# Kernel tuning notes

Hardware: AMD Instinct MI355X
Metric: run time of the kernel (lower is better)

The kernel has to match this reference:

```python
import jax, jax.numpy as jnp
from jax import lax
import numpy as np

B, T, F = 256, 2048, 12
EV_VOCAB, RS_VOCAB = 32, 8
EED, RED = 6, 3
H, K = 96, 3
D = F + EED + RED  # 21


def setup_inputs() -> dict:
    key = jax.random.key(0)
    ks = jax.random.split(key, 12)
    s = 0.05
    return {
        'seq': jax.random.normal(ks[0], (B, T, F), jnp.float32),
        'ev': jax.random.randint(ks[1], (B, T), 0, EV_VOCAB),
        'rs': jax.random.randint(ks[2], (B, T), 0, RS_VOCAB),
        'lengths': jax.random.randint(ks[3], (B,), 1, T + 1),  # valid lengths in [1, T]
        'event_emb': jax.random.normal(ks[4], (EV_VOCAB, EED), jnp.float32) * s,
        'result_emb': jax.random.normal(ks[5], (RS_VOCAB, RED), jnp.float32) * s,
        'W_ih': jax.random.normal(ks[6], (4 * H, D), jnp.float32) * s,
        'W_hh': jax.random.normal(ks[7], (4 * H, H), jnp.float32) * s,
        'b_ih': jnp.zeros((4 * H,), jnp.float32),
        'b_hh': jnp.zeros((4 * H,), jnp.float32),
        'W_mlp': jax.random.normal(ks[8], (H, H * K), jnp.float32) * s,
        'b_mlp': jnp.zeros((H,), jnp.float32),
        'W_fc': jax.random.normal(ks[9], (2, 2 * H), jnp.float32) * s,
        'b_fc': jnp.zeros((2,), jnp.float32),
    }


def reference(seq, ev, rs, lengths, event_emb, result_emb, W_ih, W_hh, b_ih, b_hh,
              W_mlp, b_mlp, W_fc, b_fc):
    # embed + concat -> [B,T,D]
    x = jnp.concatenate([seq, event_emb[ev], result_emb[rs]], axis=-1)
    xs = jnp.swapaxes(x, 0, 1)  # [T,B,D]
    ts = jnp.arange(T)
    b = b_ih + b_hh

    def step(carry, inp):
        h, c = carry
        x_t, t = inp
        gates = x_t @ W_ih.T + h @ W_hh.T + b  # [B,4H]
        i, f, g, o = jnp.split(gates, 4, axis=-1)  # PyTorch gate order i,f,g,o
        i = jax.nn.sigmoid(i); f = jax.nn.sigmoid(f)
        g = jnp.tanh(g); o = jax.nn.sigmoid(o)
        c_new = f * c + i * g
        h_new = o * jnp.tanh(c_new)
        m = (t < lengths)[:, None]  # packed-seq semantics: freeze state past length
        h = jnp.where(m, h_new, h)
        c = jnp.where(m, c_new, c)
        out = jnp.where(m, h_new, jnp.zeros_like(h_new))  # pad_packed zeros
        return (h, c), out

    h0 = jnp.zeros((B, H), x.dtype)
    (h_fin, _), outs = lax.scan(step, (h0, h0), (xs, ts))
    out_padded = jnp.swapaxes(outs, 0, 1)  # [B,T,H]

    # vectorized last-k gather (replaces torch Python loop)
    idx = lengths[:, None] - K + jnp.arange(K)  # [B,K]
    valid = idx >= 0
    gathered = jnp.take_along_axis(out_padded, jnp.clip(idx, 0)[:, :, None], axis=1)
    gathered = jnp.where(valid[:, :, None], gathered, jnp.zeros_like(gathered))
    lastk = gathered.reshape(B, K * H)

    h_lastk = jax.nn.relu(lastk @ W_mlp.T + b_mlp)
    h = jnp.concatenate([h_fin, h_lastk], axis=1)  # [B,2H]
    return h @ W_fc.T + b_fc  # [B,2]
```

## Files before the change

### kernel.cpp

```cpp
#include <hip/hip_runtime.h>

#define TT 2048
#define FF 12
#define CH 128
#define L2E 1.44269504088896340736f

typedef float v2f __attribute__((ext_vector_type(2)));

__device__ __forceinline__ float fast_exp2(float x){ return __builtin_amdgcn_exp2f(x); }
__device__ __forceinline__ float fast_rcp(float x){ return __builtin_amdgcn_rcpf(x); }
__device__ __forceinline__ v2f fma2(v2f a, v2f b, v2f c){ return __builtin_elementwise_fma(a, b, c); }
__device__ __forceinline__ v2f mk2(float x, float y){ v2f r; r.x = x; r.y = y; return r; }

__global__ __launch_bounds__(384, 2) void lstm_persist(
  const float* __restrict__ seq, const int* __restrict__ ev, const int* __restrict__ rsi,
  const int* __restrict__ len, const float* __restrict__ eemb, const float* __restrict__ remb,
  const float* __restrict__ W_ih, const float* __restrict__ W_hh,
  const float* __restrict__ b_ih, const float* __restrict__ b_hh,
  const float* __restrict__ W_mlp, const float* __restrict__ b_mlp,
  const float* __restrict__ W_fc, const float* __restrict__ b_fc,
  float* __restrict__ out)
{
  const int b   = blockIdx.x;
  const int tid = threadIdx.x;
  const int qg  = tid & 3;
  const int u   = tid >> 2;
  const int g   = qg*96 + u;

  __shared__ __align__(16) float xf[CH*24];
  __shared__ __align__(16) float vhbuf[2*96];
  __shared__ __align__(16) float lastk[3*96];
  __shared__ __align__(16) float et[192];
  __shared__ __align__(16) float rt[24];
  __shared__ __align__(16) float accs[192];
  __shared__ __align__(16) float h2[2*96];
  __shared__ int evb[CH];
  __shared__ int rsb[CH];

  v2f wh[48];
  {
    const float4* wp = (const float4*)(W_hh + g*96);
    #pragma unroll
    for (int k = 0; k < 24; ++k) {
      const float4 q4 = wp[k];
      wh[2*k]   = mk2(q4.x, q4.y);
      wh[2*k+1] = mk2(q4.z, q4.w);
    }
  }
  float wi[21];
  #pragma unroll
  for (int c = 0; c < 21; ++c) wi[c] = W_ih[g*21 + c];
  const float bg = b_ih[g] + b_hh[g];

  if (tid < 192) { vhbuf[tid] = 0.f; et[tid] = eemb[tid]; }
  if (tid < 24)  rt[tid] = remb[tid];
  if (tid < 288) lastk[tid] = 0.f;

  float c_state = 0.f;
  const int L = len[b];

  for (int t0 = 0; t0 < L; t0 += CH) {
    #pragma unroll
    for (int qq = 0; qq < 4; ++qq) {
      const int i = tid + qq*384;
      const int r = i/12, c = i - r*12;
      xf[r*24 + c] = seq[(size_t)b*(TT*FF) + (size_t)t0*FF + i];
    }
    if (tid < CH) {
      evb[tid] = ev [b*TT + t0 + tid];
      rsb[tid] = rsi[b*TT + t0 + tid];
    }
    __syncthreads();
    #pragma unroll
    for (int qq = 0; qq < 4; ++qq) {
      const int i = tid + qq*384;
      const int r = i/12, cc = i - r*12 + 12;
      float v;
      if (cc < 18)      v = et[evb[r]*6 + (cc-12)];
      else if (cc < 21) v = rt[rsb[r]*3 + (cc-18)];
      else              v = 0.f;
      xf[r*24 + cc] = v;
    }
    __syncthreads();

    const int nr = min(CH, L - t0);
    float xp;
    {
      const float* xr = xf;
      float s0 = bg, s1 = 0.f, s2 = 0.f;
      #pragma unroll
      for (int c = 0; c < 7; ++c) {
        s0 = fmaf(wi[c],    xr[c],    s0);
        s1 = fmaf(wi[c+7],  xr[c+7],  s1);
        s2 = fmaf(wi[c+14], xr[c+14], s2);
      }
      xp = s0 + s1 + s2;
    }

    for (int r = 0; r < nr; ++r) {
      const float4* hq = (const float4*)(vhbuf + (r&1)*96);
      v2f a0 = mk2(xp, 0.f), a1 = mk2(0.f,0.f), a2 = mk2(0.f,0.f), a3 = mk2(0.f,0.f);
      #pragma unroll
      for (int k = 0; k < 24; k += 2) {
        const float4 h4 = hq[k];
        const float4 h5 = hq[k+1];
        a0 = fma2(wh[2*k],   mk2(h4.x,h4.y), a0);
        a1 = fma2(wh[2*k+1], mk2(h4.z,h4.w), a1);
        a2 = fma2(wh[2*k+2], mk2(h5.x,h5.y), a2);
        a3 = fma2(wh[2*k+3], mk2(h5.z,h5.w), a3);
      }
      const float s = ((a0.x+a0.y)+(a1.x+a1.y)) + ((a2.x+a2.y)+(a3.x+a3.y));
      const bool is_t = (qg == 2);
      const float arg = is_t ? (-2.f*L2E)*fabsf(s) : (-L2E)*s;
      const float e  = fast_exp2(arg);
      const float r1 = fast_rcp(1.f + e);
      const float th = copysignf((1.f - e)*r1, s);
      const float a  = is_t ? th : r1;
      const float t1 = __shfl_xor(a, 2);
      const float t2 = __shfl_xor(a, 1);
      const float t3 = __shfl_xor(t1, 1);
      if (qg == 0) {
        c_state = fmaf(t2, c_state, a*t1);
        const float e2  = fast_exp2((-2.f*L2E)*fabsf(c_state));
        const float th2 = copysignf((1.f - e2)*fast_rcp(1.f + e2), c_state);
        const float hn  = t3 * th2;
        vhbuf[((r&1)^1)*96 + u] = hn;
        const int kk = (t0 + r) + 3 - L;
        if (kk >= 0) lastk[kk*96 + u] = hn;
      }
      if (r + 1 < nr) {
        const float* xr = xf + (r+1)*24;
        float s0 = bg, s1 = 0.f, s2 = 0.f;
        #pragma unroll
        for (int c = 0; c < 7; ++c) {
          s0 = fmaf(wi[c],    xr[c],    s0);
          s1 = fmaf(wi[c+7],  xr[c+7],  s1);
          s2 = fmaf(wi[c+14], xr[c+14], s2);
        }
        xp = s0 + s1 + s2;
      }
      __syncthreads();
    }
  }

  const float* hf = vhbuf + (L & 1)*96;
  if (tid < 192) {
    const int half = tid / 96;
    const int m    = tid - half*96;
    const float* wp = W_mlp + m*288 + half*144;
    const float* xq = lastk + half*144;
    float s = 0.f;
    #pragma unroll 8
    for (int i = 0; i < 144; ++i) s = fmaf(wp[i], xq[i], s);
    accs[tid] = s;
  }
  __syncthreads();
  if (tid < 96) {
    const float hl = accs[tid] + accs[96+tid] + b_mlp[tid];
    h2[96 + tid] = fmaxf(hl, 0.f);
    h2[tid] = hf[tid];
  }
  __syncthreads();
  if (tid < 128) {
    const int o  = tid >> 6;
    const int ll = tid & 63;
    const float* wf = W_fc + o*192 + 3*ll;
    float s = fmaf(wf[0], h2[3*ll+0], fmaf(wf[1], h2[3*ll+1], wf[2]*h2[3*ll+2]));
    #pragma unroll
    for (int off = 32; off > 0; off >>= 1) s += __shfl_down(s, off);
    if (ll == 0) out[b*2 + o] = s + b_fc[o];
  }
}

extern "C" void kernel_launch(void* const* d_in, const int* in_sizes, int n_in,
                              void* d_out, int out_size, void* d_ws, size_t ws_size,
                              hipStream_t stream) {
  const float* seq   = (const float*)d_in[0];
  const int*   ev    = (const int*)  d_in[1];
  const int*   rsi   = (const int*)  d_in[2];
  const int*   len   = (const int*)  d_in[3];
  const float* eemb  = (const float*)d_in[4];
  const float* remb  = (const float*)d_in[5];
  const float* W_ih  = (const float*)d_in[6];
  const float* W_hh  = (const float*)d_in[7];
  const float* b_ih  = (const float*)d_in[8];
  const float* b_hh  = (const float*)d_in[9];
  const float* W_mlp = (const float*)d_in[10];
  const float* b_mlp = (const float*)d_in[11];
  const float* W_fc  = (const float*)d_in[12];
  const float* b_fc  = (const float*)d_in[13];

  hipLaunchKernelGGL(lstm_persist, dim3(256), dim3(384), 0, stream,
                     seq, ev, rsi, len, eemb, remb, W_ih, W_hh, b_ih, b_hh,
                     W_mlp, b_mlp, W_fc, b_fc, (float*)d_out);
}
```

Before: 1.468 ms.

## Remap LSTM gates onto 256 threads with fused input projection

Shrinks the block from 384 to 256 threads (4 waves instead of 6). Units 0-63 each get one thread per gate, and units 64-95 are split across two threads per gate with a shuffle reduction. The input projection is folded into the recurrent dot product by appending x_t to the shared h vector and padding the weights to 120 columns. The aim is a cheaper per-step barrier across fewer waves and removal of the separate xp computation. In exchange, each thread holds up to 90 packed weight registers and does more work per step, and the critical path gains an extra shuffle.

```diff
diff --git a/kernel.cpp b/kernel.cpp
--- a/kernel.cpp
+++ b/kernel.cpp
@@ -12,7 +12,7 @@
 __device__ __forceinline__ v2f fma2(v2f a, v2f b, v2f c){ return __builtin_elementwise_fma(a, b, c); }
 __device__ __forceinline__ v2f mk2(float x, float y){ v2f r; r.x = x; r.y = y; return r; }
 
-__global__ __launch_bounds__(384, 2) void lstm_persist(
+__global__ __launch_bounds__(256, 1) void lstm_persist(
   const float* __restrict__ seq, const int* __restrict__ ev, const int* __restrict__ rsi,
   const int* __restrict__ len, const float* __restrict__ eemb, const float* __restrict__ remb,
   const float* __restrict__ W_ih, const float* __restrict__ W_hh,
@@ -24,11 +24,16 @@
   const int b   = blockIdx.x;
   const int tid = threadIdx.x;
   const int qg  = tid & 3;
-  const int u   = tid >> 2;
-  const int g   = qg*96 + u;
-
+  const int q   = tid >> 2;
+  const int oc  = tid >> 3;
+  const int s   = tid & 7;
+  const int qg2 = s >> 1;
+  const int hf  = s & 1;
+  const int gA  = qg*96  + q;
+  const int gB  = qg2*96 + 64 + oc;
+
+  __shared__ __align__(16) float vv[2][128];
   __shared__ __align__(16) float xf[CH*24];
-  __shared__ __align__(16) float vhbuf[2*96];
   __shared__ __align__(16) float lastk[3*96];
   __shared__ __align__(16) float et[192];
   __shared__ __align__(16) float rt[24];
@@ -37,32 +42,38 @@
   __shared__ int evb[CH];
   __shared__ int rsb[CH];
 
-  v2f wh[48];
-  {
-    const float4* wp = (const float4*)(W_hh + g*96);
-    #pragma unroll
-    for (int k = 0; k < 24; ++k) {
-      const float4 q4 = wp[k];
-      wh[2*k]   = mk2(q4.x, q4.y);
-      wh[2*k+1] = mk2(q4.z, q4.w);
-    }
-  }
-  float wi[21];
+  v2f wA[60];
   #pragma unroll
-  for (int c = 0; c < 21; ++c) wi[c] = W_ih[g*21 + c];
-  const float bg = b_ih[g] + b_hh[g];
-
-  if (tid < 192) { vhbuf[tid] = 0.f; et[tid] = eemb[tid]; }
+  for (int k = 0; k < 60; ++k) {
+    const int c0 = 2*k, c1 = 2*k + 1;
+    const float w0 = (c0 < 96) ? W_hh[gA*96 + c0] : ((c0 < 117) ? W_ih[gA*21 + (c0-96)] : 0.f);
+    const float w1 = (c1 < 96) ? W_hh[gA*96 + c1] : ((c1 < 117) ? W_ih[gA*21 + (c1-96)] : 0.f);
+    wA[k] = mk2(w0, w1);
+  }
+  v2f wB[30];
+  #pragma unroll
+  for (int k = 0; k < 30; ++k) {
+    const int c0 = 2*k, c1 = 2*k + 1;
+    const int d0 = hf*60 + c0, d1 = hf*60 + c1;
+    const float w0 = (d0 < 96) ? W_hh[gB*96 + d0] : ((d0 < 117) ? W_ih[gB*21 + (d0-96)] : 0.f);
+    const float w1 = (d1 < 96) ? W_hh[gB*96 + d1] : ((d1 < 117) ? W_ih[gB*21 + (d1-96)] : 0.f);
+    wB[k] = mk2(w0, w1);
+  }
+  const float bgA = b_ih[gA] + b_hh[gA];
+  const float bgB = (hf == 0) ? (b_ih[gB] + b_hh[gB]) : 0.f;
+
+  ((float*)vv)[tid] = 0.f;
+  if (tid < 192) et[tid] = eemb[tid];
   if (tid < 24)  rt[tid] = remb[tid];
-  if (tid < 288) lastk[tid] = 0.f;
-
-  float c_state = 0.f;
+  for (int i = tid; i < 288; i += 256) lastk[i] = 0.f;
+
+  float cA = 0.f, cB = 0.f;
   const int L = len[b];
 
   for (int t0 = 0; t0 < L; t0 += CH) {
     #pragma unroll
-    for (int qq = 0; qq < 4; ++qq) {
-      const int i = tid + qq*384;
+    for (int qq = 0; qq < 6; ++qq) {
+      const int i = tid + qq*256;
       const int r = i/12, c = i - r*12;
       xf[r*24 + c] = seq[(size_t)b*(TT*FF) + (size_t)t0*FF + i];
     }
@@ -72,8 +83,8 @@
     }
     __syncthreads();
     #pragma unroll
-    for (int qq = 0; qq < 4; ++qq) {
-      const int i = tid + qq*384;
+    for (int qq = 0; qq < 6; ++qq) {
+      const int i = tid + qq*256;
       const int r = i/12, cc = i - r*12 + 12;
       float v;
       if (cc < 18)      v = et[evb[r]*6 + (cc-12)];
@@ -82,93 +93,99 @@
       xf[r*24 + cc] = v;
     }
     __syncthreads();
+    if (tid < 24) vv[0][96 + tid] = xf[tid];
+    __syncthreads();
 
     const int nr = min(CH, L - t0);
-    float xp;
-    {
-      const float* xr = xf;
-      float s0 = bg, s1 = 0.f, s2 = 0.f;
+    for (int r = 0; r < nr; ++r) {
+      const int p = r & 1;
+      const float4* va = (const float4*)(vv[p]);
+      const float4* vb = (const float4*)(vv[p] + hf*60);
+
+      v2f a0 = mk2(bgA, 0.f), a1 = mk2(0.f,0.f), a2 = mk2(0.f,0.f), a3 = mk2(0.f,0.f);
+      v2f bb0 = mk2(bgB, 0.f), bb1 = mk2(0.f,0.f);
       #pragma unroll
-      for (int c = 0; c < 7; ++c) {
-        s0 = fmaf(wi[c],    xr[c],    s0);
-        s1 = fmaf(wi[c+7],  xr[c+7],  s1);
-        s2 = fmaf(wi[c+14], xr[c+14], s2);
+      for (int k = 0; k < 15; ++k) {
+        const float4 x0 = va[2*k];
+        const float4 x1 = va[2*k+1];
+        const float4 y0 = vb[k];
+        a0  = fma2(wA[4*k+0], mk2(x0.x,x0.y), a0);
+        a1  = fma2(wA[4*k+1], mk2(x0.z,x0.w), a1);
+        a2  = fma2(wA[4*k+2], mk2(x1.x,x1.y), a2);
+        a3  = fma2(wA[4*k+3], mk2(x1.z,x1.w), a3);
+        bb0 = fma2(wB[2*k+0], mk2(y0.x,y0.y), bb0);
+        bb1 = fma2(wB[2*k+1], mk2(y0.z,y0.w), bb1);
       }
-      xp = s0 + s1 + s2;
-    }
-
-    for (int r = 0; r < nr; ++r) {
-      const float4* hq = (const float4*)(vhbuf + (r&1)*96);
-      v2f a0 = mk2(xp, 0.f), a1 = mk2(0.f,0.f), a2 = mk2(0.f,0.f), a3 = mk2(0.f,0.f);
-      #pragma unroll
-      for (int k = 0; k < 24; k += 2) {
-        const float4 h4 = hq[k];
-        const float4 h5 = hq[k+1];
-        a0 = fma2(wh[2*k],   mk2(h4.x,h4.y), a0);
-        a1 = fma2(wh[2*k+1], mk2(h4.z,h4.w), a1);
-        a2 = fma2(wh[2*k+2], mk2(h5.x,h5.y), a2);
-        a3 = fma2(wh[2*k+3], mk2(h5.z,h5.w), a3);
+      const v2f sa = (a0 + a1) + (a2 + a3);
+      const float sA = sa.x + sa.y;
+      const v2f sb = bb0 + bb1;
+      float sB = sb.x + sb.y;
+      sB += __shfl_xor(sB, 1);
+
+      const bool tA = (qg == 2);
+      const float eA = fast_exp2(tA ? (-2.f*L2E)*fabsf(sA) : (-L2E)*sA);
+      const float rA = fast_rcp(1.f + eA);
+      const float aA = tA ? copysignf((1.f - eA)*rA, sA) : rA;
+      const bool tB = (qg2 == 2);
+      const float eB = fast_exp2(tB ? (-2.f*L2E)*fabsf(sB) : (-L2E)*sB);
+      const float rB = fast_rcp(1.f + eB);
+      const float aB = tB ? copysignf((1.f - eB)*rB, sB) : rB;
+
+      const float fA_ = __shfl_xor(aA, 1);
+      const float gA_ = __shfl_xor(aA, 2);
+      const float oA_ = __shfl_xor(fA_, 2);
+      const float fB_ = __shfl_xor(aB, 2);
+      const float gB_ = __shfl_xor(aB, 4);
+      const float oB_ = __shfl_xor(fB_, 4);
+
+      const int kk = (t0 + r) + 3 - L;
+      if (qg == 0) {
+        cA = fmaf(fA_, cA, aA * gA_);
+        const float e2 = fast_exp2((-2.f*L2E)*fabsf(cA));
+        const float th = copysignf((1.f - e2)*fast_rcp(1.f + e2), cA);
+        const float hn = oA_ * th;
+        vv[p^1][q] = hn;
+        if (kk >= 0) lastk[kk*96 + q] = hn;
       }
-      const float s = ((a0.x+a0.y)+(a1.x+a1.y)) + ((a2.x+a2.y)+(a3.x+a3.y));
-      const bool is_t = (qg == 2);
-      const float arg = is_t ? (-2.f*L2E)*fabsf(s) : (-L2E)*s;
-      const float e  = fast_exp2(arg);
-      const float r1 = fast_rcp(1.f + e);
-      const float th = copysignf((1.f - e)*r1, s);
-      const float a  = is_t ? th : r1;
-      const float t1 = __shfl_xor(a, 2);
-      const float t2 = __shfl_xor(a, 1);
-      const float t3 = __shfl_xor(t1, 1);
-      if (qg == 0) {
-        c_state = fmaf(t2, c_state, a*t1);
-        const float e2  = fast_exp2((-2.f*L2E)*fabsf(c_state));
-        const float th2 = copysignf((1.f - e2)*fast_rcp(1.f + e2), c_state);
-        const float hn  = t3 * th2;
-        vhbuf[((r&1)^1)*96 + u] = hn;
-        const int kk = (t0 + r) + 3 - L;
-        if (kk >= 0) lastk[kk*96 + u] = hn;
+      if (s == 0) {
+        cB = fmaf(fB_, cB, aB * gB_);
+        const float e2 = fast_exp2((-2.f*L2E)*fabsf(cB));
+        const float th = copysignf((1.f - e2)*fast_rcp(1.f + e2), cB);
+        const float hn = oB_ * th;
+        vv[p^1][64 + oc] = hn;
+        if (kk >= 0) lastk[kk*96 + 64 + oc] = hn;
       }
-      if (r + 1 < nr) {
-        const float* xr = xf + (r+1)*24;
-        float s0 = bg, s1 = 0.f, s2 = 0.f;
-        #pragma unroll
-        for (int c = 0; c < 7; ++c) {
-          s0 = fmaf(wi[c],    xr[c],    s0);
-          s1 = fmaf(wi[c+7],  xr[c+7],  s1);
-          s2 = fmaf(wi[c+14], xr[c+14], s2);
-        }
-        xp = s0 + s1 + s2;
-      }
+      if (qg == 1 && q < 24 && r + 1 < nr) vv[p^1][96 + q] = xf[(r+1)*24 + q];
       __syncthreads();
     }
   }
 
-  const float* hf = vhbuf + (L & 1)*96;
+  const float* hfin = vv[L & 1];
   if (tid < 192) {
     const int half = tid / 96;
     const int m    = tid - half*96;
     const float* wp = W_mlp + m*288 + half*144;
     const float* xq = lastk + half*144;
-    float s = 0.f;
+    float ssum = 0.f;
     #pragma unroll 8
-    for (int i = 0; i < 144; ++i) s = fmaf(wp[i], xq[i], s);
-    accs[tid] = s;
+    for (int i = 0; i < 144; ++i) ssum = fmaf(wp[i], xq[i], ssum);
+    accs[tid] = ssum;
   }
   __syncthreads();
   if (tid < 96) {
     const float hl = accs[tid] + accs[96+tid] + b_mlp[tid];
     h2[96 + tid] = fmaxf(hl, 0.f);
-    h2[tid] = hf[tid];
+    h2[tid] = hfin[tid];
   }
   __syncthreads();
   if (tid < 128) {
     const int o  = tid >> 6;
     const int ll = tid & 63;
     const float* wf = W_fc + o*192 + 3*ll;
-    float s = fmaf(wf[0], h2[3*ll+0], fmaf(wf[1], h2[3*ll+1], wf[2]*h2[3*ll+2]));
+    float ssum = fmaf(wf[0], h2[3*ll+0], fmaf(wf[1], h2[3*ll+1], wf[2]*h2[3*ll+2]));
     #pragma unroll
-    for (int off = 32; off > 0; off >>= 1) s += __shfl_down(s, off);
-    if (ll == 0) out[b*2 + o] = s + b_fc[o];
+    for (int off = 32; off > 0; off >>= 1) ssum += __shfl_down(ssum, off);
+    if (ll == 0) out[b*2 + o] = ssum + b_fc[o];
   }
 }
 
@@ -190,7 +207,7 @@
   const float* W_fc  = (const float*)d_in[12];
   const float* b_fc  = (const float*)d_in[13];
 
-  hipLaunchKernelGGL(lstm_persist, dim3(256), dim3(384), 0, stream,
+  hipLaunchKernelGGL(lstm_persist, dim3(256), dim3(256), 0, stream,
                      seq, ev, rsi, len, eemb, remb, W_ih, W_hh, b_ih, b_hh,
                      W_mlp, b_mlp, W_fc, b_fc, (float*)d_out);
 }
```

Result: slower. 1.989 ms (+35.5%).
